# Kernel optimization log

Measured on AMD Instinct MI355X. Metric: run time of the kernel, lower is better.

## Reference

```python
import jax, jax.numpy as jnp
import numpy as np

D = 256      # input_size == output_size
H = 8        # head_count
DH = D // H  # dim per head


def setup_inputs() -> dict:
    key = jax.random.key(0)
    ks = jax.random.split(key, 11)
    s = 1.0 / np.sqrt(D)
    inp = {
        "x": jax.random.normal(ks[0], (4, 2048, D), dtype=jnp.float32),
        "Wq": jax.random.normal(ks[1], (D, D), dtype=jnp.float32) * s,
        "bq": jnp.zeros((D,), jnp.float32),
        "Wk": jax.random.normal(ks[2], (D, D), dtype=jnp.float32) * s,
        "bk": jnp.zeros((D,), jnp.float32),
        "Wv": jax.random.normal(ks[3], (D, D), dtype=jnp.float32) * s,
        "bv": jnp.zeros((D,), jnp.float32),
        "Wo": jax.random.normal(ks[4], (D, D), dtype=jnp.float32) * s,
        "bo": jnp.zeros((D,), jnp.float32),
        "Wc": jax.random.normal(ks[5], (D, D), dtype=jnp.float32) * s,
        "bc": jnp.zeros((D,), jnp.float32),
    }
    return inp


def _split_heads(t):
    b, n, _ = t.shape
    return t.reshape(b, n, H, DH).transpose(0, 2, 1, 3)  # b h n dh


def reference(x, Wq, bq, Wk, bk, Wv, bv, Wo, bo, Wc, bc):
    # Multi-head self-attention over all nodes (complete graph)
    q = _split_heads(x @ Wq + bq)
    k = _split_heads(x @ Wk + bk)
    v = _split_heads(x @ Wv + bv)
    scale = 1.0 / jnp.sqrt(jnp.asarray(DH, x.dtype))
    scores = jnp.einsum("bhqd,bhkd->bhqk", q * scale, k)
    attn = jax.nn.softmax(scores, axis=-1)  # attn dropout = identity (eval)
    ctx = jnp.einsum("bhqk,bhkd->bhqd", attn, v)
    b, _, n, _ = ctx.shape
    ctx = ctx.transpose(0, 2, 1, 3).reshape(b, n, D)
    ctx = ctx @ Wo + bo  # MHA output projection
    # linear_context + dropout (identity in eval) + residual
    out = x + (ctx @ Wc + bc)
    return out
```

## Files before the change

kernel.cpp:

```cpp
#include <hip/hip_runtime.h>

#define DMODEL 256
#define HEADS 8
#define DHEAD 32
#define NSEQ 2048
#define BATCH 4
#define MTOT (BATCH*NSEQ)

typedef __bf16 bf16x8 __attribute__((ext_vector_type(8)));
typedef float f32x4 __attribute__((ext_vector_type(4)));

#define CS 0.25507282111989365f

__device__ __forceinline__ unsigned short f2bf(float f) {
    union { float f; unsigned int u; } v; v.f = f;
    unsigned int u = v.u;
    unsigned int r = u + 0x7FFFu + ((u >> 16) & 1u);
    return (unsigned short)(r >> 16);
}

__device__ __forceinline__ unsigned pkbf(float a, float b) {
    union { __bf16 h[2]; unsigned u; } t;
    t.h[0] = (__bf16)a; t.h[1] = (__bf16)b;
    return t.u;
}

__device__ __forceinline__ f32x4 mfma16(bf16x8 a, bf16x8 b, f32x4 c) {
    return __builtin_amdgcn_mfma_f32_16x16x32_bf16(a, b, c, 0, 0, 0);
}

#define GLD16(g, l) __builtin_amdgcn_global_load_lds( \
    (const __attribute__((address_space(1))) unsigned int*)(g), \
    (__attribute__((address_space(3))) unsigned int*)(l), 16, 0, 0)

__global__ __launch_bounds__(256) void prep_kernel(
    const float* __restrict__ x,
    const float* __restrict__ Wq, const float* __restrict__ Wk,
    const float* __restrict__ Wv, const float* __restrict__ Wo,
    const float* __restrict__ Wc,
    const float* __restrict__ bq, const float* __restrict__ bk,
    const float* __restrict__ bv, const float* __restrict__ bo,
    const float* __restrict__ bc,
    unsigned short* __restrict__ xbf,
    unsigned short* __restrict__ Wt,
    float* __restrict__ bcat,
    unsigned short* __restrict__ Woct,
    float* __restrict__ bocf)
{
    if (blockIdx.x < 257) {
        int k = blockIdx.x;
        int n = threadIdx.x;
        const float* arow = (k < 256) ? (Wo + k * 256) : bo;
        float a0 = 0.f, a1 = 0.f, a2 = 0.f, a3 = 0.f;
#pragma unroll 4
        for (int j = 0; j < 256; j += 4) {
            a0 = fmaf(arow[j],     Wc[j * 256 + n],       a0);
            a1 = fmaf(arow[j + 1], Wc[(j + 1) * 256 + n], a1);
            a2 = fmaf(arow[j + 2], Wc[(j + 2) * 256 + n], a2);
            a3 = fmaf(arow[j + 3], Wc[(j + 3) * 256 + n], a3);
        }
        float acc = (a0 + a1) + (a2 + a3);
        if (k < 256) Woct[n * 256 + k] = f2bf(acc);
        else         bocf[n] = acc + bc[n];
        return;
    }
    int idx = (blockIdx.x - 257) * 256 + threadIdx.x;
    const int nx4 = (MTOT * DMODEL) / 4;
    if (idx < nx4) {
        float4 v = reinterpret_cast<const float4*>(x)[idx];
        ushort4 o;
        o.x = f2bf(v.x); o.y = f2bf(v.y); o.z = f2bf(v.z); o.w = f2bf(v.w);
        reinterpret_cast<ushort4*>(xbf)[idx] = o;
        return;
    }
    int t = idx - nx4;
    if (t < 1280 * 256) {
        int n = t >> 8, k = t & 255;
        const float* Wsrc; int col;
        if (n < 256)       { Wsrc = Wq; col = n; }
        else if (n < 512)  { Wsrc = Wk; col = n - 256; }
        else if (n < 768)  { Wsrc = Wv; col = n - 512; }
        else if (n < 1024) { Wsrc = Wo; col = n - 768; }
        else               { Wsrc = Wc; col = n - 1024; }
        Wt[t] = f2bf(Wsrc[k * 256 + col]);
        return;
    }
    t -= 1280 * 256;
    if (t < 1280) {
        float v;
        if (t < 256)       v = bq[t];
        else if (t < 512)  v = bk[t - 256];
        else if (t < 768)  v = bv[t - 512];
        else if (t < 1024) v = bo[t - 768];
        else               v = bc[t - 1024];
        bcat[t] = v;
    }
}

template<int MODE, int WM>
__global__ __launch_bounds__(WM * 64) void gemm32(
    const unsigned short* __restrict__ A,
    const unsigned short* __restrict__ Wt,
    const float* __restrict__ bias,
    const float* __restrict__ xres,
    unsigned short* __restrict__ outQ,
    unsigned short* __restrict__ outK,
    unsigned short* __restrict__ outVt,
    float* __restrict__ outF)
{
    __shared__ __align__(16) unsigned short Bl[64 * 256];
    const int tid = threadIdx.x;
    const int wid = tid >> 6;
    const int lane = tid & 63;
    const int lo = lane & 15, hi = lane >> 4;
    const int m0 = blockIdx.x * (WM * 32) + wid * 32;
    const int n0 = blockIdx.y * 64;

    const int NCALL = 2048 / (WM * 64);
#pragma unroll
    for (int j = 0; j < NCALL; ++j) {
        int chunkbase = (j * WM + wid) * 64;
        int chunk = chunkbase + lane;
        int row = chunk >> 5, Jp = chunk & 31;
        int J = (Jp & 24) | ((Jp ^ row) & 7);
        GLD16(Wt + (n0 + row) * 256 + J * 8, Bl + chunkbase * 8);
    }
    asm volatile("s_waitcnt vmcnt(0)" ::: "memory");
    __syncthreads();

    const unsigned short* arow0 = A + (m0 + lo) * 256 + hi * 8;
    f32x4 acc[2][4] = {};
#pragma unroll
    for (int s = 0; s < 8; ++s) {
        bf16x8 a0 = *reinterpret_cast<const bf16x8*>(arow0 + s * 32);
        bf16x8 a1 = *reinterpret_cast<const bf16x8*>(arow0 + 16 * 256 + s * 32);
        int Jp = ((s >> 1) << 3) | ((((s & 1) << 2) + hi) ^ (lo & 7));
#pragma unroll
        for (int n = 0; n < 4; ++n) {
            bf16x8 b = *reinterpret_cast<const bf16x8*>(
                Bl + (n * 16 + lo) * 256 + Jp * 8);
            acc[0][n] = mfma16(a0, b, acc[0][n]);
            acc[1][n] = mfma16(a1, b, acc[1][n]);
        }
    }

    if (MODE == 2) {
#pragma unroll
        for (int mf = 0; mf < 2; ++mf) {
            const int row_base = m0 + mf * 16 + hi * 4;
#pragma unroll
            for (int n = 0; n < 4; ++n) {
                int gc = n0 + n * 16 + lo;
                float bs = bias[gc];
#pragma unroll
                for (int i = 0; i < 4; ++i)
                    outF[(row_base + i) * 256 + gc] =
                        xres[(row_base + i) * 256 + gc] + acc[mf][n][i] + bs;
            }
        }
        return;
    }

    const int type = blockIdx.y >> 2;
    const int m0b = blockIdx.x * 128;
    unsigned short* Lb = Bl;
    __syncthreads();
    if (type < 2) {
#pragma unroll
        for (int mf = 0; mf < 2; ++mf)
#pragma unroll
        for (int n = 0; n < 4; ++n) {
            float bs = bias[n0 + n * 16 + lo];
#pragma unroll
            for (int i = 0; i < 4; ++i) {
                float val = acc[mf][n][i] + bs;
                if (type == 0) val *= CS;
                Lb[(wid * 32 + mf * 16 + hi * 4 + i) * 72 + n * 16 + lo] = f2bf(val);
            }
        }
    } else {
#pragma unroll
        for (int mf = 0; mf < 2; ++mf)
#pragma unroll
        for (int n = 0; n < 4; ++n) {
            float bs = bias[n0 + n * 16 + lo];
            uint2 pk;
            pk.x = pkbf(acc[mf][n][0] + bs, acc[mf][n][1] + bs);
            pk.y = pkbf(acc[mf][n][2] + bs, acc[mf][n][3] + bs);
            *reinterpret_cast<uint2*>(
                Lb + (n * 16 + lo) * 136 + wid * 32 + mf * 16 + hi * 4) = pk;
        }
    }
    __syncthreads();
    if (type < 2) {
        unsigned short* outP = (type == 0) ? outQ : outK;
#pragma unroll
        for (int r = 0; r < 4; ++r) {
            int cid = r * 256 + tid;
            int m_l = cid >> 3, seg = cid & 7;
            bf16x8 chunk = *reinterpret_cast<const bf16x8*>(Lb + m_l * 72 + seg * 8);
            int m = m0b + m_l, gc = n0 + seg * 8;
            int b = m >> 11, nn = m & 2047, hh = (gc >> 5) & 7, dh = gc & 31;
            *reinterpret_cast<bf16x8*>(
                outP + (((b * 8) + hh) * 2048 + nn) * 32 + dh) = chunk;
        }
    } else {
#pragma unroll
        for (int r = 0; r < 4; ++r) {
            int cid = r * 256 + tid;
            int gcl = cid >> 4, seg = cid & 15;
            bf16x8 chunk = *reinterpret_cast<const bf16x8*>(Lb + gcl * 136 + seg * 8);
            int gc = n0 + gcl, m = m0b + seg * 8;
            int b = m >> 11, nn = m & 2047, hh = (gc >> 5) & 7, dh = gc & 31;
            *reinterpret_cast<bf16x8*>(
                outVt + (((b * 8) + hh) * 32 + dh) * 2048 + nn) = chunk;
        }
    }
}

__global__ __launch_bounds__(512, 4) void attn_kernel(
    const unsigned short* __restrict__ Q,
    const unsigned short* __restrict__ K,
    const unsigned short* __restrict__ Vt,
    unsigned short* __restrict__ ctx)
{
    __shared__ __align__(16) char smem[65536];

    const int tid = threadIdx.x;
    const int wid = tid >> 6;
    const int lane = tid & 63;
    const int lo = lane & 15, hi = lane >> 4;
    const int half = wid >> 2;
    const int qw = wid & 3;

    const int bid = blockIdx.x;
    const int bh = ((bid >> 7) << 3) | (bid & 7);
    const int qt = (bid >> 3) & 15;
    const int q0 = qt * 128 + qw * 32;

    const unsigned short* Qb = Q + bh * (NSEQ * 32);
    const unsigned short* Kb = K + bh * (NSEQ * 32);
    const unsigned short* Vb = Vt + bh * (32 * NSEQ);

    bf16x8 qfA = *reinterpret_cast<const bf16x8*>(Qb + (q0 + lo) * 32 + hi * 8);
    bf16x8 qfB = *reinterpret_cast<const bf16x8*>(Qb + (q0 + 16 + lo) * 32 + hi * 8);

    const int lt = tid & 255;
    const int kb0 = half * 1024;
    const unsigned short* ksrc0 = Kb + (kb0 + 2 * (lt >> 3) + ((lt >> 2) & 1)) * 32
                                     + ((lt & 3) ^ ((lt >> 3) & 3)) * 8;
    const unsigned short* ksrc1 = ksrc0 + 64 * 32;
    const unsigned short* vsrc0 = Vb + (lt >> 3) * NSEQ + kb0
                                     + ((lt & 7) ^ ((lt >> 3) & 7)) * 8;
    const unsigned short* vsrc1 = vsrc0 + 64;
    char* kdst = smem + half * 16384 + lt * 16;
    char* vdst = smem + 32768 + half * 16384 + lt * 16;

    f32x4 o0A = {}, o1A = {}, odA = {};
    f32x4 o0B = {}, o1B = {}, odB = {};
    const f32x4 z = {};
    const int prs = lo & 7;
    const int kxor = (hi ^ ((lo >> 1) & 3)) * 8;

    union { unsigned u[4]; bf16x8 v; } ones;
    ones.u[0] = 0x3F803F80u; ones.u[1] = 0x3F803F80u;
    ones.u[2] = 0x3F803F80u; ones.u[3] = 0x3F803F80u;

#define STAGE_T(tt, buf) do { \
    GLD16(ksrc0 + (tt) * 4096, kdst + (buf) * 8192); \
    GLD16(ksrc1 + (tt) * 4096, kdst + (buf) * 8192 + 4096); \
    GLD16(vsrc0 + (tt) * 128,  vdst + (buf) * 8192); \
    GLD16(vsrc1 + (tt) * 128,  vdst + (buf) * 8192 + 4096); \
} while (0)

    STAGE_T(0, 0);
    asm volatile("s_waitcnt vmcnt(0)" ::: "memory");
    __builtin_amdgcn_s_barrier();
    __builtin_amdgcn_sched_barrier(0);

    int cur = 0;
    for (int t = 0; t < 8; ++t) {
        if (t < 7) STAGE_T(t + 1, cur ^ 1);
        const unsigned short* Kc =
            (const unsigned short*)(smem + half * 16384 + cur * 8192);
        const unsigned short* Vc =
            (const unsigned short*)(smem + 32768 + half * 16384 + cur * 8192);

        __builtin_amdgcn_s_setprio(1);
#pragma unroll
        for (int h2 = 0; h2 < 2; ++h2) {
            const unsigned short* Kh = Kc + h2 * 2048;
            const unsigned short* Vh = Vc + h2 * 2048;
            f32x4 sA[4], sB[4];
#pragma unroll
            for (int c = 0; c < 4; ++c) {
                bf16x8 kf = *reinterpret_cast<const bf16x8*>(
                    Kh + (c * 16 + lo) * 32 + kxor);
                sA[c] = mfma16(kf, qfA, z);
                sB[c] = mfma16(kf, qfB, z);
            }
#pragma unroll
            for (int kk = 0; kk < 2; ++kk) {
                unsigned uA = pkbf(__builtin_amdgcn_exp2f(sA[2 * kk][0]),
                                   __builtin_amdgcn_exp2f(sA[2 * kk][1]));
                unsigned uB = pkbf(__builtin_amdgcn_exp2f(sA[2 * kk][2]),
                                   __builtin_amdgcn_exp2f(sA[2 * kk][3]));
                unsigned uC = pkbf(__builtin_amdgcn_exp2f(sA[2 * kk + 1][0]),
                                   __builtin_amdgcn_exp2f(sA[2 * kk + 1][1]));
                unsigned uD = pkbf(__builtin_amdgcn_exp2f(sA[2 * kk + 1][2]),
                                   __builtin_amdgcn_exp2f(sA[2 * kk + 1][3]));
                auto r1 = __builtin_amdgcn_permlane32_swap(uA, uC, false, false);
                auto r2 = __builtin_amdgcn_permlane16_swap(r1[0], r1[1], false, false);
                auto r3 = __builtin_amdgcn_permlane32_swap(uB, uD, false, false);
                auto r4 = __builtin_amdgcn_permlane16_swap(r3[0], r3[1], false, false);
                union { unsigned u[4]; bf16x8 v; } pbA;
                pbA.u[0] = r2[0]; pbA.u[1] = r4[0]; pbA.u[2] = r2[1]; pbA.u[3] = r4[1];
                unsigned wA = pkbf(__builtin_amdgcn_exp2f(sB[2 * kk][0]),
                                   __builtin_amdgcn_exp2f(sB[2 * kk][1]));
                unsigned wB = pkbf(__builtin_amdgcn_exp2f(sB[2 * kk][2]),
                                   __builtin_amdgcn_exp2f(sB[2 * kk][3]));
                unsigned wC = pkbf(__builtin_amdgcn_exp2f(sB[2 * kk + 1][0]),
                                   __builtin_amdgcn_exp2f(sB[2 * kk + 1][1]));
                unsigned wD = pkbf(__builtin_amdgcn_exp2f(sB[2 * kk + 1][2]),
                                   __builtin_amdgcn_exp2f(sB[2 * kk + 1][3]));
                auto t1 = __builtin_amdgcn_permlane32_swap(wA, wC, false, false);
                auto t2 = __builtin_amdgcn_permlane16_swap(t1[0], t1[1], false, false);
                auto t3 = __builtin_amdgcn_permlane32_swap(wB, wD, false, false);
                auto t4 = __builtin_amdgcn_permlane16_swap(t3[0], t3[1], false, false);
                union { unsigned u[4]; bf16x8 v; } pbB;
                pbB.u[0] = t2[0]; pbB.u[1] = t4[0]; pbB.u[2] = t2[1]; pbB.u[3] = t4[1];

                int sw = ((4 * kk + hi) ^ prs) * 8;
                bf16x8 a0 = *reinterpret_cast<const bf16x8*>(Vh + lo * 64 + sw);
                bf16x8 a1 = *reinterpret_cast<const bf16x8*>(Vh + (16 + lo) * 64 + sw);
                o0A = mfma16(a0, pbA.v, o0A);
                o1A = mfma16(a1, pbA.v, o1A);
                odA = mfma16(ones.v, pbA.v, odA);
                o0B = mfma16(a0, pbB.v, o0B);
                o1B = mfma16(a1, pbB.v, o1B);
                odB = mfma16(ones.v, pbB.v, odB);
            }
        }
        __builtin_amdgcn_s_setprio(0);

        if (t < 7) {
            asm volatile("s_waitcnt vmcnt(0)" ::: "memory");
            __builtin_amdgcn_s_barrier();
            __builtin_amdgcn_sched_barrier(0);
            cur ^= 1;
        }
    }

    float* comb = (float*)smem;
    const int cidx = (qw * 64 + lane) * 18;
    __syncthreads();
    if (half) {
        *reinterpret_cast<f32x4*>(comb + cidx)      = o0A;
        *reinterpret_cast<f32x4*>(comb + cidx + 4)  = o1A;
        comb[cidx + 8] = odA[0];
        *reinterpret_cast<f32x4*>(comb + cidx + 9)  = o0B;
        *reinterpret_cast<f32x4*>(comb + cidx + 13) = o1B;
        comb[cidx + 17] = odB[0];
    }
    __syncthreads();
    if (!half) {
        o0A += *reinterpret_cast<const f32x4*>(comb + cidx);
        o1A += *reinterpret_cast<const f32x4*>(comb + cidx + 4);
        float invA = 1.0f / (odA[0] + comb[cidx + 8]);
        o0B += *reinterpret_cast<const f32x4*>(comb + cidx + 9);
        o1B += *reinterpret_cast<const f32x4*>(comb + cidx + 13);
        float invB = 1.0f / (odB[0] + comb[cidx + 17]);

        const int b = bh >> 3, h = bh & 7;
        unsigned short* dstA = ctx + (size_t)((b * 2048 + q0 + lo)) * 256 + h * 32;
        unsigned short* dstB = dstA + 16 * 256;
        ushort4 w0, w1;
        w0.x = f2bf(o0A[0] * invA); w0.y = f2bf(o0A[1] * invA);
        w0.z = f2bf(o0A[2] * invA); w0.w = f2bf(o0A[3] * invA);
        w1.x = f2bf(o1A[0] * invA); w1.y = f2bf(o1A[1] * invA);
        w1.z = f2bf(o1A[2] * invA); w1.w = f2bf(o1A[3] * invA);
        *reinterpret_cast<ushort4*>(dstA + hi * 4)      = w0;
        *reinterpret_cast<ushort4*>(dstA + 16 + hi * 4) = w1;
        w0.x = f2bf(o0B[0] * invB); w0.y = f2bf(o0B[1] * invB);
        w0.z = f2bf(o0B[2] * invB); w0.w = f2bf(o0B[3] * invB);
        w1.x = f2bf(o1B[0] * invB); w1.y = f2bf(o1B[1] * invB);
        w1.z = f2bf(o1B[2] * invB); w1.w = f2bf(o1B[3] * invB);
        *reinterpret_cast<ushort4*>(dstB + hi * 4)      = w0;
        *reinterpret_cast<ushort4*>(dstB + 16 + hi * 4) = w1;
    }
#undef STAGE_T
}

extern "C" void kernel_launch(void* const* d_in, const int* in_sizes, int n_in,
                              void* d_out, int out_size, void* d_ws, size_t ws_size,
                              hipStream_t stream) {
    const float* x  = (const float*)d_in[0];
    const float* Wq = (const float*)d_in[1];
    const float* bq = (const float*)d_in[2];
    const float* Wk = (const float*)d_in[3];
    const float* bk = (const float*)d_in[4];
    const float* Wv = (const float*)d_in[5];
    const float* bv = (const float*)d_in[6];
    const float* Wo = (const float*)d_in[7];
    const float* bo = (const float*)d_in[8];
    const float* Wc = (const float*)d_in[9];
    const float* bc = (const float*)d_in[10];
    float* out = (float*)d_out;

    char* p = (char*)d_ws;
    unsigned short* xbf  = (unsigned short*)p;  p += (size_t)MTOT * DMODEL * 2;
    unsigned short* Wt   = (unsigned short*)p;  p += (size_t)1280 * 256 * 2;
    float* bcat          = (float*)p;           p += (size_t)1280 * 4;
    unsigned short* Qw   = (unsigned short*)p;  p += (size_t)32 * 2048 * 32 * 2;
    unsigned short* Kw   = (unsigned short*)p;  p += (size_t)32 * 2048 * 32 * 2;
    unsigned short* Vtw  = (unsigned short*)p;  p += (size_t)32 * 32 * 2048 * 2;
    unsigned short* ctx  = (unsigned short*)p;  p += (size_t)MTOT * DMODEL * 2;
    unsigned short* Woct = (unsigned short*)p;  p += (size_t)256 * 256 * 2;
    float* bocf          = (float*)p;           p += (size_t)256 * 4;

    prep_kernel<<<3590, 256, 0, stream>>>(x, Wq, Wk, Wv, Wo, Wc,
                                          bq, bk, bv, bo, bc,
                                          xbf, Wt, bcat, Woct, bocf);
    gemm32<0, 4><<<dim3(64, 12), 256, 0, stream>>>(xbf, Wt, bcat, nullptr,
                                                   Qw, Kw, Vtw, nullptr);
    attn_kernel<<<512, 512, 0, stream>>>(Qw, Kw, Vtw, ctx);
    gemm32<2, 4><<<dim3(64, 4), 256, 0, stream>>>(ctx, Woct, bocf,
                                                  x, nullptr, nullptr, nullptr, out);
}
```

Measured before the change: 62.80 us.

## Fuse x cast into QKV GEMM, split attention KV halves across blocks

The separate x-to-bf16 conversion pass is removed; the QKV GEMM now loads fp32 x directly and packs to bf16 in registers. The weight transpose in prep is rewritten as a tiled LDS transpose with fewer blocks. Attention now launches twice as many 256-thread blocks, each handling one half of the keys, and writes unnormalized fp32 partial outputs and denominators to global memory. The output GEMM then combines and normalizes the two halves while loading its A operand. This trades the in-block LDS combine and bf16 ctx for extra fp32 global traffic (two full partial buffers) in exchange for more attention parallelism and one fewer full-tensor pass.

```diff
diff --git a/kernel.cpp b/kernel.cpp
--- a/kernel.cpp
+++ b/kernel.cpp
@@ -34,22 +34,45 @@
     (__attribute__((address_space(3))) unsigned int*)(l), 16, 0, 0)
 
 __global__ __launch_bounds__(256) void prep_kernel(
-    const float* __restrict__ x,
     const float* __restrict__ Wq, const float* __restrict__ Wk,
     const float* __restrict__ Wv, const float* __restrict__ Wo,
     const float* __restrict__ Wc,
     const float* __restrict__ bq, const float* __restrict__ bk,
     const float* __restrict__ bv, const float* __restrict__ bo,
     const float* __restrict__ bc,
-    unsigned short* __restrict__ xbf,
     unsigned short* __restrict__ Wt,
     float* __restrict__ bcat,
     unsigned short* __restrict__ Woct,
     float* __restrict__ bocf)
 {
-    if (blockIdx.x < 257) {
-        int k = blockIdx.x;
-        int n = threadIdx.x;
+    const int tid = threadIdx.x;
+    if (blockIdx.x < 80) {
+        __shared__ unsigned short Lt[64 * 72];
+        const int wid = tid >> 6, lane = tid & 63;
+        const int n0 = (blockIdx.x >> 2) * 64, k0 = (blockIdx.x & 3) * 64;
+        const float* Wsrc; int col0;
+        if (n0 < 256)       { Wsrc = Wq; col0 = n0; }
+        else if (n0 < 512)  { Wsrc = Wk; col0 = n0 - 256; }
+        else if (n0 < 768)  { Wsrc = Wv; col0 = n0 - 512; }
+        else if (n0 < 1024) { Wsrc = Wo; col0 = n0 - 768; }
+        else                { Wsrc = Wc; col0 = n0 - 1024; }
+#pragma unroll
+        for (int r = 0; r < 16; ++r) {
+            int k = k0 + wid * 16 + r;
+            Lt[lane * 72 + wid * 16 + r] = f2bf(Wsrc[k * 256 + col0 + lane]);
+        }
+        __syncthreads();
+#pragma unroll
+        for (int c = tid; c < 512; c += 256) {
+            int row = c >> 3, seg = c & 7;
+            *reinterpret_cast<bf16x8*>(Wt + (n0 + row) * 256 + k0 + seg * 8) =
+                *reinterpret_cast<const bf16x8*>(Lt + row * 72 + seg * 8);
+        }
+        return;
+    }
+    if (blockIdx.x < 337) {
+        int k = blockIdx.x - 80;
+        int n = tid;
         const float* arow = (k < 256) ? (Wo + k * 256) : bo;
         float a0 = 0.f, a1 = 0.f, a2 = 0.f, a3 = 0.f;
 #pragma unroll 4
@@ -64,28 +87,7 @@
         else         bocf[n] = acc + bc[n];
         return;
     }
-    int idx = (blockIdx.x - 257) * 256 + threadIdx.x;
-    const int nx4 = (MTOT * DMODEL) / 4;
-    if (idx < nx4) {
-        float4 v = reinterpret_cast<const float4*>(x)[idx];
-        ushort4 o;
-        o.x = f2bf(v.x); o.y = f2bf(v.y); o.z = f2bf(v.z); o.w = f2bf(v.w);
-        reinterpret_cast<ushort4*>(xbf)[idx] = o;
-        return;
-    }
-    int t = idx - nx4;
-    if (t < 1280 * 256) {
-        int n = t >> 8, k = t & 255;
-        const float* Wsrc; int col;
-        if (n < 256)       { Wsrc = Wq; col = n; }
-        else if (n < 512)  { Wsrc = Wk; col = n - 256; }
-        else if (n < 768)  { Wsrc = Wv; col = n - 512; }
-        else if (n < 1024) { Wsrc = Wo; col = n - 768; }
-        else               { Wsrc = Wc; col = n - 1024; }
-        Wt[t] = f2bf(Wsrc[k * 256 + col]);
-        return;
-    }
-    t -= 1280 * 256;
+    int t = (blockIdx.x - 337) * 256 + tid;
     if (t < 1280) {
         float v;
         if (t < 256)       v = bq[t];
@@ -97,29 +99,25 @@
     }
 }
 
-template<int MODE, int WM>
-__global__ __launch_bounds__(WM * 64) void gemm32(
-    const unsigned short* __restrict__ A,
+__global__ __launch_bounds__(256) void gemm_qkv(
+    const float* __restrict__ X,
     const unsigned short* __restrict__ Wt,
     const float* __restrict__ bias,
-    const float* __restrict__ xres,
     unsigned short* __restrict__ outQ,
     unsigned short* __restrict__ outK,
-    unsigned short* __restrict__ outVt,
-    float* __restrict__ outF)
+    unsigned short* __restrict__ outVt)
 {
     __shared__ __align__(16) unsigned short Bl[64 * 256];
     const int tid = threadIdx.x;
     const int wid = tid >> 6;
     const int lane = tid & 63;
     const int lo = lane & 15, hi = lane >> 4;
-    const int m0 = blockIdx.x * (WM * 32) + wid * 32;
+    const int m0 = blockIdx.x * 128 + wid * 32;
     const int n0 = blockIdx.y * 64;
 
-    const int NCALL = 2048 / (WM * 64);
-#pragma unroll
-    for (int j = 0; j < NCALL; ++j) {
-        int chunkbase = (j * WM + wid) * 64;
+#pragma unroll
+    for (int j = 0; j < 8; ++j) {
+        int chunkbase = (j * 4 + wid) * 64;
         int chunk = chunkbase + lane;
         int row = chunk >> 5, Jp = chunk & 31;
         int J = (Jp & 24) | ((Jp ^ row) & 7);
@@ -128,37 +126,27 @@
     asm volatile("s_waitcnt vmcnt(0)" ::: "memory");
     __syncthreads();
 
-    const unsigned short* arow0 = A + (m0 + lo) * 256 + hi * 8;
+    const float* arow0 = X + (m0 + lo) * 256 + hi * 8;
     f32x4 acc[2][4] = {};
 #pragma unroll
     for (int s = 0; s < 8; ++s) {
-        bf16x8 a0 = *reinterpret_cast<const bf16x8*>(arow0 + s * 32);
-        bf16x8 a1 = *reinterpret_cast<const bf16x8*>(arow0 + 16 * 256 + s * 32);
+        float4 xa = *reinterpret_cast<const float4*>(arow0 + s * 32);
+        float4 xb = *reinterpret_cast<const float4*>(arow0 + s * 32 + 4);
+        float4 ya = *reinterpret_cast<const float4*>(arow0 + 16 * 256 + s * 32);
+        float4 yb = *reinterpret_cast<const float4*>(arow0 + 16 * 256 + s * 32 + 4);
+        union { unsigned u[4]; bf16x8 v; } a0, a1;
+        a0.u[0] = pkbf(xa.x, xa.y); a0.u[1] = pkbf(xa.z, xa.w);
+        a0.u[2] = pkbf(xb.x, xb.y); a0.u[3] = pkbf(xb.z, xb.w);
+        a1.u[0] = pkbf(ya.x, ya.y); a1.u[1] = pkbf(ya.z, ya.w);
+        a1.u[2] = pkbf(yb.x, yb.y); a1.u[3] = pkbf(yb.z, yb.w);
         int Jp = ((s >> 1) << 3) | ((((s & 1) << 2) + hi) ^ (lo & 7));
 #pragma unroll
         for (int n = 0; n < 4; ++n) {
             bf16x8 b = *reinterpret_cast<const bf16x8*>(
                 Bl + (n * 16 + lo) * 256 + Jp * 8);
-            acc[0][n] = mfma16(a0, b, acc[0][n]);
-            acc[1][n] = mfma16(a1, b, acc[1][n]);
-        }
-    }
-
-    if (MODE == 2) {
-#pragma unroll
-        for (int mf = 0; mf < 2; ++mf) {
-            const int row_base = m0 + mf * 16 + hi * 4;
-#pragma unroll
-            for (int n = 0; n < 4; ++n) {
-                int gc = n0 + n * 16 + lo;
-                float bs = bias[gc];
-#pragma unroll
-                for (int i = 0; i < 4; ++i)
-                    outF[(row_base + i) * 256 + gc] =
-                        xres[(row_base + i) * 256 + gc] + acc[mf][n][i] + bs;
-            }
-        }
-        return;
+            acc[0][n] = mfma16(a0.v, b, acc[0][n]);
+            acc[1][n] = mfma16(a1.v, b, acc[1][n]);
+        }
     }
 
     const int type = blockIdx.y >> 2;
@@ -218,25 +206,25 @@
     }
 }
 
-__global__ __launch_bounds__(512, 4) void attn_kernel(
+__global__ __launch_bounds__(256, 4) void attn_kernel(
     const unsigned short* __restrict__ Q,
     const unsigned short* __restrict__ K,
     const unsigned short* __restrict__ Vt,
-    unsigned short* __restrict__ ctx)
+    float* __restrict__ Op,
+    float* __restrict__ dp)
 {
-    __shared__ __align__(16) char smem[65536];
+    __shared__ __align__(16) char smem[32768];
 
     const int tid = threadIdx.x;
     const int wid = tid >> 6;
     const int lane = tid & 63;
     const int lo = lane & 15, hi = lane >> 4;
-    const int half = wid >> 2;
-    const int qw = wid & 3;
 
     const int bid = blockIdx.x;
-    const int bh = ((bid >> 7) << 3) | (bid & 7);
-    const int qt = (bid >> 3) & 15;
-    const int q0 = qt * 128 + qw * 32;
+    const int r = bid & 7, tq = bid >> 3;
+    const int qt = tq & 15, half = (tq >> 4) & 1, g = tq >> 5;
+    const int bh = g * 8 + r;
+    const int q0 = qt * 128 + wid * 32;
 
     const unsigned short* Qb = Q + bh * (NSEQ * 32);
     const unsigned short* Kb = K + bh * (NSEQ * 32);
@@ -245,7 +233,7 @@
     bf16x8 qfA = *reinterpret_cast<const bf16x8*>(Qb + (q0 + lo) * 32 + hi * 8);
     bf16x8 qfB = *reinterpret_cast<const bf16x8*>(Qb + (q0 + 16 + lo) * 32 + hi * 8);
 
-    const int lt = tid & 255;
+    const int lt = tid;
     const int kb0 = half * 1024;
     const unsigned short* ksrc0 = Kb + (kb0 + 2 * (lt >> 3) + ((lt >> 2) & 1)) * 32
                                      + ((lt & 3) ^ ((lt >> 3) & 3)) * 8;
@@ -253,8 +241,8 @@
     const unsigned short* vsrc0 = Vb + (lt >> 3) * NSEQ + kb0
                                      + ((lt & 7) ^ ((lt >> 3) & 7)) * 8;
     const unsigned short* vsrc1 = vsrc0 + 64;
-    char* kdst = smem + half * 16384 + lt * 16;
-    char* vdst = smem + 32768 + half * 16384 + lt * 16;
+    char* kdst = smem + lt * 16;
+    char* vdst = smem + 16384 + lt * 16;
 
     f32x4 o0A = {}, o1A = {}, odA = {};
     f32x4 o0B = {}, o1B = {}, odB = {};
@@ -281,10 +269,8 @@
     int cur = 0;
     for (int t = 0; t < 8; ++t) {
         if (t < 7) STAGE_T(t + 1, cur ^ 1);
-        const unsigned short* Kc =
-            (const unsigned short*)(smem + half * 16384 + cur * 8192);
-        const unsigned short* Vc =
-            (const unsigned short*)(smem + 32768 + half * 16384 + cur * 8192);
+        const unsigned short* Kc = (const unsigned short*)(smem + cur * 8192);
+        const unsigned short* Vc = (const unsigned short*)(smem + 16384 + cur * 8192);
 
         __builtin_amdgcn_s_setprio(1);
 #pragma unroll
@@ -315,6 +301,7 @@
                 auto r4 = __builtin_amdgcn_permlane16_swap(r3[0], r3[1], false, false);
                 union { unsigned u[4]; bf16x8 v; } pbA;
                 pbA.u[0] = r2[0]; pbA.u[1] = r4[0]; pbA.u[2] = r2[1]; pbA.u[3] = r4[1];
+
                 unsigned wA = pkbf(__builtin_amdgcn_exp2f(sB[2 * kk][0]),
                                    __builtin_amdgcn_exp2f(sB[2 * kk][1]));
                 unsigned wB = pkbf(__builtin_amdgcn_exp2f(sB[2 * kk][2]),
@@ -351,44 +338,100 @@
         }
     }
 
-    float* comb = (float*)smem;
-    const int cidx = (qw * 64 + lane) * 18;
+    const int b = bh >> 3, h = bh & 7;
+    float* OpH = Op + (size_t)half * 2097152
+                    + (size_t)(b * 2048 + q0 + lo) * 256 + h * 32;
+    *reinterpret_cast<f32x4*>(OpH + hi * 4)             = o0A;
+    *reinterpret_cast<f32x4*>(OpH + 16 + hi * 4)        = o1A;
+    *reinterpret_cast<f32x4*>(OpH + 16 * 256 + hi * 4)      = o0B;
+    *reinterpret_cast<f32x4*>(OpH + 16 * 256 + 16 + hi * 4) = o1B;
+    if (hi == 0) {
+        float* dpH = dp + half * 65536 + bh * 2048 + q0;
+        dpH[lo]      = odA[0];
+        dpH[16 + lo] = odB[0];
+    }
+#undef STAGE_T
+}
+
+__global__ __launch_bounds__(256) void gemm_out(
+    const float* __restrict__ Op,
+    const float* __restrict__ dp,
+    const unsigned short* __restrict__ Wt,
+    const float* __restrict__ boc,
+    const float* __restrict__ xres,
+    float* __restrict__ outF)
+{
+    __shared__ __align__(16) unsigned short Bl[64 * 256];
+    const int tid = threadIdx.x;
+    const int wid = tid >> 6;
+    const int lane = tid & 63;
+    const int lo = lane & 15, hi = lane >> 4;
+    const int m0 = blockIdx.x * 128 + wid * 32;
+    const int n0 = blockIdx.y * 64;
+
+#pragma unroll
+    for (int j = 0; j < 8; ++j) {
+        int chunkbase = (j * 4 + wid) * 64;
+        int chunk = chunkbase + lane;
+        int row = chunk >> 5, Jp = chunk & 31;
+        int J = (Jp & 24) | ((Jp ^ row) & 7);
+        GLD16(Wt + (n0 + row) * 256 + J * 8, Bl + chunkbase * 8);
+    }
+    asm volatile("s_waitcnt vmcnt(0)" ::: "memory");
     __syncthreads();
-    if (half) {
-        *reinterpret_cast<f32x4*>(comb + cidx)      = o0A;
-        *reinterpret_cast<f32x4*>(comb + cidx + 4)  = o1A;
-        comb[cidx + 8] = odA[0];
-        *reinterpret_cast<f32x4*>(comb + cidx + 9)  = o0B;
-        *reinterpret_cast<f32x4*>(comb + cidx + 13) = o1B;
-        comb[cidx + 17] = odB[0];
-    }
-    __syncthreads();
-    if (!half) {
-        o0A += *reinterpret_cast<const f32x4*>(comb + cidx);
-        o1A += *reinterpret_cast<const f32x4*>(comb + cidx + 4);
-        float invA = 1.0f / (odA[0] + comb[cidx + 8]);
-        o0B += *reinterpret_cast<const f32x4*>(comb + cidx + 9);
-        o1B += *reinterpret_cast<const f32x4*>(comb + cidx + 13);
-        float invB = 1.0f / (odB[0] + comb[cidx + 17]);
-
-        const int b = bh >> 3, h = bh & 7;
-        unsigned short* dstA = ctx + (size_t)((b * 2048 + q0 + lo)) * 256 + h * 32;
-        unsigned short* dstB = dstA + 16 * 256;
-        ushort4 w0, w1;
-        w0.x = f2bf(o0A[0] * invA); w0.y = f2bf(o0A[1] * invA);
-        w0.z = f2bf(o0A[2] * invA); w0.w = f2bf(o0A[3] * invA);
-        w1.x = f2bf(o1A[0] * invA); w1.y = f2bf(o1A[1] * invA);
-        w1.z = f2bf(o1A[2] * invA); w1.w = f2bf(o1A[3] * invA);
-        *reinterpret_cast<ushort4*>(dstA + hi * 4)      = w0;
-        *reinterpret_cast<ushort4*>(dstA + 16 + hi * 4) = w1;
-        w0.x = f2bf(o0B[0] * invB); w0.y = f2bf(o0B[1] * invB);
-        w0.z = f2bf(o0B[2] * invB); w0.w = f2bf(o0B[3] * invB);
-        w1.x = f2bf(o1B[0] * invB); w1.y = f2bf(o1B[1] * invB);
-        w1.z = f2bf(o1B[2] * invB); w1.w = f2bf(o1B[3] * invB);
-        *reinterpret_cast<ushort4*>(dstB + hi * 4)      = w0;
-        *reinterpret_cast<ushort4*>(dstB + 16 + hi * 4) = w1;
-    }
-#undef STAGE_T
+
+    const int mA = m0 + lo;
+    const float* op0 = Op + (size_t)mA * 256 + hi * 8;
+    const int b0 = mA >> 11, nn0 = mA & 2047;
+    const int b1 = (mA + 16) >> 11, nn1 = (mA + 16) & 2047;
+    const float* db0 = dp + b0 * 16384 + nn0;
+    const float* db1 = dp + b1 * 16384 + nn1;
+
+    f32x4 acc[2][4] = {};
+#pragma unroll
+    for (int s = 0; s < 8; ++s) {
+        float d0 = db0[s * 2048] + db0[65536 + s * 2048];
+        float d1 = db1[s * 2048] + db1[65536 + s * 2048];
+        float i0 = 1.0f / d0, i1 = 1.0f / d1;
+        f32x4 pa = *reinterpret_cast<const f32x4*>(op0 + s * 32);
+        f32x4 pb = *reinterpret_cast<const f32x4*>(op0 + s * 32 + 4);
+        f32x4 qa = *reinterpret_cast<const f32x4*>(op0 + 2097152 + s * 32);
+        f32x4 qb = *reinterpret_cast<const f32x4*>(op0 + 2097152 + s * 32 + 4);
+        f32x4 ra = *reinterpret_cast<const f32x4*>(op0 + 16 * 256 + s * 32);
+        f32x4 rb = *reinterpret_cast<const f32x4*>(op0 + 16 * 256 + s * 32 + 4);
+        f32x4 sa = *reinterpret_cast<const f32x4*>(op0 + 2097152 + 16 * 256 + s * 32);
+        f32x4 sb = *reinterpret_cast<const f32x4*>(op0 + 2097152 + 16 * 256 + s * 32 + 4);
+        union { unsigned u[4]; bf16x8 v; } a0, a1;
+        a0.u[0] = pkbf((pa[0] + qa[0]) * i0, (pa[1] + qa[1]) * i0);
+        a0.u[1] = pkbf((pa[2] + qa[2]) * i0, (pa[3] + qa[3]) * i0);
+        a0.u[2] = pkbf((pb[0] + qb[0]) * i0, (pb[1] + qb[1]) * i0);
+        a0.u[3] = pkbf((pb[2] + qb[2]) * i0, (pb[3] + qb[3]) * i0);
+        a1.u[0] = pkbf((ra[0] + sa[0]) * i1, (ra[1] + sa[1]) * i1);
+        a1.u[1] = pkbf((ra[2] + sa[2]) * i1, (ra[3] + sa[3]) * i1);
+        a1.u[2] = pkbf((rb[0] + sb[0]) * i1, (rb[1] + sb[1]) * i1);
+        a1.u[3] = pkbf((rb[2] + sb[2]) * i1, (rb[3] + sb[3]) * i1);
+        int Jp = ((s >> 1) << 3) | ((((s & 1) << 2) + hi) ^ (lo & 7));
+#pragma unroll
+        for (int n = 0; n < 4; ++n) {
+            bf16x8 bfr = *reinterpret_cast<const bf16x8*>(
+                Bl + (n * 16 + lo) * 256 + Jp * 8);
+            acc[0][n] = mfma16(a0.v, bfr, acc[0][n]);
+            acc[1][n] = mfma16(a1.v, bfr, acc[1][n]);
+        }
+    }
+#pragma unroll
+    for (int mf = 0; mf < 2; ++mf) {
+        const int row_base = m0 + mf * 16 + hi * 4;
+#pragma unroll
+        for (int n = 0; n < 4; ++n) {
+            int gc = n0 + n * 16 + lo;
+            float bs = boc[gc];
+#pragma unroll
+            for (int i = 0; i < 4; ++i)
+                outF[(row_base + i) * 256 + gc] =
+                    xres[(row_base + i) * 256 + gc] + acc[mf][n][i] + bs;
+        }
+    }
 }
 
 extern "C" void kernel_launch(void* const* d_in, const int* in_sizes, int n_in,
@@ -408,22 +451,20 @@
     float* out = (float*)d_out;
 
     char* p = (char*)d_ws;
-    unsigned short* xbf  = (unsigned short*)p;  p += (size_t)MTOT * DMODEL * 2;
     unsigned short* Wt   = (unsigned short*)p;  p += (size_t)1280 * 256 * 2;
     float* bcat          = (float*)p;           p += (size_t)1280 * 4;
     unsigned short* Qw   = (unsigned short*)p;  p += (size_t)32 * 2048 * 32 * 2;
     unsigned short* Kw   = (unsigned short*)p;  p += (size_t)32 * 2048 * 32 * 2;
     unsigned short* Vtw  = (unsigned short*)p;  p += (size_t)32 * 32 * 2048 * 2;
-    unsigned short* ctx  = (unsigned short*)p;  p += (size_t)MTOT * DMODEL * 2;
+    float* Opart         = (float*)p;           p += (size_t)2 * MTOT * 256 * 4;
+    float* dpart         = (float*)p;           p += (size_t)2 * 32 * 2048 * 4;
     unsigned short* Woct = (unsigned short*)p;  p += (size_t)256 * 256 * 2;
     float* bocf          = (float*)p;           p += (size_t)256 * 4;
 
-    prep_kernel<<<3590, 256, 0, stream>>>(x, Wq, Wk, Wv, Wo, Wc,
-                                          bq, bk, bv, bo, bc,
-                                          xbf, Wt, bcat, Woct, bocf);
-    gemm32<0, 4><<<dim3(64, 12), 256, 0, stream>>>(xbf, Wt, bcat, nullptr,
-                                                   Qw, Kw, Vtw, nullptr);
-    attn_kernel<<<512, 512, 0, stream>>>(Qw, Kw, Vtw, ctx);
-    gemm32<2, 4><<<dim3(64, 4), 256, 0, stream>>>(ctx, Woct, bocf,
-                                                  x, nullptr, nullptr, nullptr, out);
-}
+    prep_kernel<<<342, 256, 0, stream>>>(Wq, Wk, Wv, Wo, Wc,
+                                         bq, bk, bv, bo, bc,
+                                         Wt, bcat, Woct, bocf);
+    gemm_qkv<<<dim3(64, 12), 256, 0, stream>>>(x, Wt, bcat, Qw, Kw, Vtw);
+    attn_kernel<<<1024, 256, 0, stream>>>(Qw, Kw, Vtw, Opart, dpart);
+    gemm_out<<<dim3(64, 4), 256, 0, stream>>>(Opart, dpart, Woct, bocf, x, out);
+}
```

Result: slower. 84.60 us (+34.7%).
